# Kernel tuning notes

Hardware: AMD Instinct MI355X
Metric: run time of the kernel (lower is better)

The kernel has to match this reference:

```python
import jax, jax.numpy as jnp
import numpy as np

K = 20
EPS = 1e-5

def get_graph_feature(x, k):
    # x: [B, C, N] -> edge features [B, 2C, N, k]
    xt = jnp.swapaxes(x, 1, 2)  # [B, N, C]
    sq = jnp.sum(xt * xt, axis=-1)  # [B, N]
    # negative squared distance: -(|a|^2 + |b|^2 - 2 a.b)
    pair = 2.0 * jnp.einsum('bnc,bmc->bnm', xt, xt) - sq[:, :, None] - sq[:, None, :]
    idx = jax.lax.top_k(pair, k)[1]  # [B, N, k] nearest neighbors (incl. self)
    neigh = jax.vmap(lambda f, i: f[i])(xt, idx)  # [B, N, k, C]
    ctr = xt[:, :, None, :]  # [B, N, 1, C]
    edge = jnp.concatenate([neigh - ctr, jnp.broadcast_to(ctr, neigh.shape)], axis=-1)  # [B,N,k,2C]
    return jnp.transpose(edge, (0, 3, 1, 2))  # [B, 2C, N, k]

def bn_lrelu(y, g, b, axes):
    # training-mode batchnorm (biased batch stats) + LeakyReLU(0.2)
    m = jnp.mean(y, axis=axes, keepdims=True)
    v = jnp.var(y, axis=axes, keepdims=True)
    shape = [1, -1] + [1] * (y.ndim - 2)
    yn = (y - m) / jnp.sqrt(v + EPS) * g.reshape(shape) + b.reshape(shape)
    return jnp.where(yn >= 0, yn, 0.2 * yn)

def edge_block(x, w, g, b, k):
    e = get_graph_feature(x, k)           # [B, 2C, N, k]
    y = jnp.einsum('bcnk,oc->bonk', e, w)  # 1x1 conv2d, no bias
    y = bn_lrelu(y, g, b, (0, 2, 3))
    return jnp.max(y, axis=-1)            # max over k -> [B, O, N]

def setup_inputs() -> dict:
    key = jax.random.key(0)
    ks = jax.random.split(key, 8)
    B, N = 8, 1024
    num_features = 256
    def w(k_, o, i):
        return jax.random.normal(k_, (o, i), dtype=jnp.float32) * (1.0 / np.sqrt(i))
    d = {
        'x': jax.random.normal(ks[0], (B, N, 3), dtype=jnp.float32),
        'w1': w(ks[1], 64, 6),   'g1': jnp.ones(64),  'b1': jnp.zeros(64),
        'w2': w(ks[2], 64, 128), 'g2': jnp.ones(64),  'b2': jnp.zeros(64),
        'w3': w(ks[3], 128, 128),'g3': jnp.ones(128), 'b3': jnp.zeros(128),
        'w4': w(ks[4], 256, 256),'g4': jnp.ones(256), 'b4': jnp.zeros(256),
        'w5': w(ks[5], 512, 512),'g5': jnp.ones(512), 'b5': jnp.zeros(512),
        'wemb': w(ks[6], num_features, 512),
    }
    return d

def reference(x, w1, g1, b1, w2, g2, b2, w3, g3, b3, w4, g4, b4, w5, g5, b5, wemb):
    xc = jnp.swapaxes(x, 2, 1)  # [B, 3, N]
    x1 = edge_block(xc, w1, g1, b1, K)  # [B, 64, N]
    x2 = edge_block(x1, w2, g2, b2, K)  # [B, 64, N]
    x3 = edge_block(x2, w3, g3, b3, K)  # [B, 128, N]
    x4 = edge_block(x3, w4, g4, b4, K)  # [B, 256, N]
    cat = jnp.concatenate([x1, x2, x3, x4], axis=1)  # [B, 512, N]
    y = jnp.einsum('bcn,oc->bon', cat, w5)            # 1x1 conv1d
    y = bn_lrelu(y, g5, b5, (0, 2))
    feat = jnp.max(y, axis=-1)  # [B, 512]
    return feat @ wemb.T        # [B, num_features]
```

## Files before the change

### kernel.cpp

```cpp
#include <hip/hip_runtime.h>
#include <hip/hip_bf16.h>
#include <math.h>

#define BB 8
#define NN 1024
#define KNNK 20
#define LDC 512

typedef __attribute__((ext_vector_type(8))) short bfrag8;
typedef __attribute__((ext_vector_type(4))) float facc4;
typedef __attribute__((ext_vector_type(2))) float v2f;

struct bh8 { __hip_bfloat16 h[8]; };

__device__ __forceinline__ bh8 cvt8(float4 a, float4 b) {
    bh8 v;
    v.h[0] = __float2bfloat16(a.x); v.h[1] = __float2bfloat16(a.y);
    v.h[2] = __float2bfloat16(a.z); v.h[3] = __float2bfloat16(a.w);
    v.h[4] = __float2bfloat16(b.x); v.h[5] = __float2bfloat16(b.y);
    v.h[6] = __float2bfloat16(b.z); v.h[7] = __float2bfloat16(b.w);
    return v;
}

template<int CTRL, int RMASK>
__device__ __forceinline__ float fmax_dpp(float x) {
    int xi = __float_as_int(x);
    int yi = __builtin_amdgcn_update_dpp(xi, xi, CTRL, RMASK, 0xF, false);
    return fmaxf(x, __int_as_float(yi));
}

__device__ __forceinline__ float wave_max64(float x) {
    x = fmax_dpp<0x121, 0xF>(x);
    x = fmax_dpp<0x122, 0xF>(x);
    x = fmax_dpp<0x124, 0xF>(x);
    x = fmax_dpp<0x128, 0xF>(x);
    x = fmax_dpp<0x142, 0xA>(x);
    x = fmax_dpp<0x143, 0xC>(x);
    return __int_as_float(__builtin_amdgcn_readlane(__float_as_int(x), 63));
}

__device__ __forceinline__ void select20_pf(float (*dist)[1024],
                                            int q0, int w, int lane,
                                            int* __restrict__ idxout) {
    float d[2][16];
    int   sl[2][16];
#pragma unroll
    for (int qi = 0; qi < 2; qi++) {
        int row = w * 2 + qi;
#pragma unroll
        for (int j = 0; j < 16; j++) { d[qi][j] = dist[row][lane + 64 * j]; sl[qi][j] = j; }
    }
    constexpr unsigned char CA[63] = {
        0,2,4,6,8,10,12,14,
        0,1,4,5,8,9,12,13,
        1,5,9,13,
        0,1,2,3,8,9,10,11,
        2,3,10,11,
        1,3,5,9,11,13,
        0,1,2,3,4,5,6,7,
        4,5,6,7,
        2,3,6,7,10,11,
        1,3,5,7,9,11,13};
    constexpr unsigned char CB[63] = {
        1,3,5,7,9,11,13,15,
        2,3,6,7,10,11,14,15,
        2,6,10,14,
        4,5,6,7,12,13,14,15,
        4,5,12,13,
        2,4,6,10,12,14,
        8,9,10,11,12,13,14,15,
        8,9,10,11,
        4,5,8,9,12,13,
        2,4,6,8,10,12,14};
#pragma unroll
    for (int c = 0; c < 63; c++) {
        const int a = CA[c], bq = CB[c];
#pragma unroll
        for (int qi = 0; qi < 2; qi++) {
            bool sw = d[qi][a] < d[qi][bq];
            float dmx = sw ? d[qi][bq] : d[qi][a];
            float dmn = sw ? d[qi][a]  : d[qi][bq];
            d[qi][a] = dmx; d[qi][bq] = dmn;
            int smx = sw ? sl[qi][bq] : sl[qi][a];
            int smn = sw ? sl[qi][a]  : sl[qi][bq];
            sl[qi][a] = smx; sl[qi][bq] = smn;
        }
    }
    unsigned long long slp[2];
#pragma unroll
    for (int qi = 0; qi < 2; qi++) {
        int row = w * 2 + qi;
#pragma unroll
        for (int j = 0; j < 16; j++) dist[row][j * 64 + lane] = d[qi][j];
        unsigned long long p = 0;
#pragma unroll
        for (int j = 0; j < 16; j++) p |= (unsigned long long)sl[qi][j] << (4 * j);
        slp[qi] = p;
    }
    float head[2] = {d[0][0], d[1][0]};
    float pf[2]   = {d[0][1], d[1][1]};
    int   ptr[2]  = {2, 2};
    for (int t = 0; t < KNNK; t++) {
#pragma unroll
        for (int qi = 0; qi < 2; qi++) {
            int row = w * 2 + qi;
            float bv = wave_max64(head[qi]);
            unsigned long long ball = __ballot(head[qi] == bv);
            int wl = (int)__builtin_ctzll(ball);
            bool win = (lane == wl);
            if (win) {
                idxout[(q0 + row) * KNNK + t] = (int)(slp[qi] & 15ull) * 64 + lane;
            }
            head[qi] = win ? pf[qi] : head[qi];
            slp[qi]  = win ? (slp[qi] >> 4) : slp[qi];
            if (win) {
                int p = ptr[qi];
                pf[qi] = (p < 16) ? dist[row][p * 64 + lane] : -INFINITY;
                ptr[qi] = p + 1;
            }
        }
    }
}

__device__ __forceinline__ void zero_r1(float* r1s, float* r1q, int O, int tid) {
    for (int i = tid; i < 32 * O; i += 256) { r1s[i] = 0.f; r1q[i] = 0.f; }
}

__global__ __launch_bounds__(256, 4) void knn3_fused(const float* __restrict__ x,
                                                     const float* __restrict__ w1,
                                                     float* __restrict__ zf,
                                                     int* __restrict__ idxout,
                                                     float* __restrict__ r1s, float* __restrict__ r1q) {
    __shared__ float dist[8][1024];
    int tid = threadIdx.x;
    int q0 = (blockIdx.x & 7) * 1024 + (blockIdx.x >> 3) * 8;
    int b = q0 >> 10;
    if (blockIdx.x == 0) zero_r1(r1s, r1q, 64, tid);
    const float* xb = x + (size_t)b * NN * 3;
    int lane = tid & 63, w = tid >> 6;
    float qx[8], qy[8], qz[8];
#pragma unroll
    for (int q = 0; q < 8; q++) {
        const float* qr = xb + (size_t)((q0 & (NN - 1)) + q) * 3;
        qx[q] = qr[0]; qy[q] = qr[1]; qz[q] = qr[2];
    }
#pragma unroll
    for (int cq = 0; cq < 4; cq++) {
        int cand = w * 256 + cq * 64 + lane;
        const float* cr = xb + (size_t)cand * 3;
        float cx = cr[0], cy = cr[1], cz = cr[2];
        float sqc = cx * cx + cy * cy + cz * cz;
#pragma unroll
        for (int q = 0; q < 8; q++) {
            float d = qx[q] * cx + qy[q] * cy + qz[q] * cz;
            dist[q][cand] = 2.f * d - sqc;
        }
    }
    for (int i = tid; i < 8 * 128; i += 256) {
        int lq = i >> 7, j = i & 127;
        const float* wr = w1 + (j < 64 ? j * 6 : (j - 64) * 6 + 3);
        const float* xr = x + (size_t)(q0 + lq) * 3;
        zf[(size_t)(q0 + lq) * 128 + j] = wr[0] * xr[0] + wr[1] * xr[1] + wr[2] * xr[2];
    }
    __syncthreads();
    select20_pf(dist, q0, w, lane, idxout);
}

template<int C>
__device__ __forceinline__ void knn_body(const float* __restrict__ xT,
                                         const float* __restrict__ sqn,
                                         int* __restrict__ idxout,
                                         float (*dist)[1024], int knnBlk) {
    int tid = threadIdx.x;
    int q0 = (knnBlk & 7) * 1024 + (knnBlk >> 3) * 8;
    int b = q0 >> 10;
    int lane = tid & 63, w = tid >> 6;
    int cand0 = w * 256 + 4 * lane;
    const float* xTb = xT + (size_t)b * C * 1024;
    const float* qrow = xTb + (q0 & (NN - 1));
    float4 sq4 = *(const float4*)(sqn + b * NN + cand0);
    v2f acc2[4][4];
#pragma unroll
    for (int j = 0; j < 4; j++)
#pragma unroll
        for (int p = 0; p < 4; p++) acc2[j][p] = (v2f){0.f, 0.f};
    for (int cg = 0; cg < C / 4; cg++) {
        float4 rch[4];
#pragma unroll
        for (int c = 0; c < 4; c++)
            rch[c] = *(const float4*)(xTb + (size_t)(4 * cg + c) * 1024 + cand0);
#pragma unroll
        for (int c = 0; c < 4; c++) {
            const float* qr = qrow + (size_t)(4 * cg + c) * 1024;
            float4 qa = *(const float4*)qr;
            float4 qb = *(const float4*)(qr + 4);
            v2f qp[4] = {{qa.x, qa.y}, {qa.z, qa.w}, {qb.x, qb.y}, {qb.z, qb.w}};
            float rj[4] = {rch[c].x, rch[c].y, rch[c].z, rch[c].w};
#pragma unroll
            for (int j = 0; j < 4; j++) {
                v2f rr = {rj[j], rj[j]};
                acc2[j][0] += rr * qp[0];
                acc2[j][1] += rr * qp[1];
                acc2[j][2] += rr * qp[2];
                acc2[j][3] += rr * qp[3];
            }
        }
    }
#pragma unroll
    for (int p = 0; p < 4; p++)
#pragma unroll
        for (int half = 0; half < 2; half++) {
            int q = 2 * p + half;
            float4 dv;
            dv.x = 2.f * acc2[0][p][half] - sq4.x;
            dv.y = 2.f * acc2[1][p][half] - sq4.y;
            dv.z = 2.f * acc2[2][p][half] - sq4.z;
            dv.w = 2.f * acc2[3][p][half] - sq4.w;
            *(float4*)&dist[q][cand0] = dv;
        }
    __syncthreads();
    select20_pf(dist, q0, w, lane, idxout);
}

template<int C, int ZO2>
__global__ __launch_bounds__(256, 4) void knnz_fat(const float* __restrict__ xT,
                                                   const float* __restrict__ xt, int off,
                                                   const float* __restrict__ sqn,
                                                   int* __restrict__ idxout,
                                                   const float* __restrict__ w,
                                                   float* __restrict__ zf,
                                                   float* __restrict__ r1s, float* __restrict__ r1q,
                                                   int Onext) {
    __shared__ float dist[8][1024];
    int tid = threadIdx.x;
    if ((int)blockIdx.x < BB * NN / 8) {
        knn_body<C>(xT, sqn, idxout, dist, blockIdx.x);
        return;
    }
    constexpr int ZO = ZO2 / 2;
    int zblk = blockIdx.x - BB * NN / 8;
    if (zblk == 0) zero_r1(r1s, r1q, Onext, tid);
    float (*xs)[C] = (float (*)[C])&dist[0][0];
    int p0 = zblk * 16;
    for (int j = tid; j < 16 * (C / 4); j += 256) {
        int p = j / (C / 4), c4 = j % (C / 4);
        *(float4*)&xs[p][4 * c4] = *(const float4*)(xt + (size_t)(p0 + p) * LDC + off + 4 * c4);
    }
    __syncthreads();
    for (int j = tid; j < ZO2; j += 256) {
        const float* wr = w + (j < ZO ? (size_t)j * 2 * C : (size_t)(j - ZO) * 2 * C + C);
        float acc[16];
#pragma unroll
        for (int p = 0; p < 16; p++) acc[p] = 0.f;
        for (int c4 = 0; c4 < C / 4; c4++) {
            float4 wv = *(const float4*)(wr + 4 * c4);
#pragma unroll
            for (int p = 0; p < 16; p++) {
                float4 xv = *(const float4*)&xs[p][4 * c4];
                acc[p] += wv.x * xv.x + wv.y * xv.y + wv.z * xv.z + wv.w * xv.w;
            }
        }
#pragma unroll
        for (int p = 0; p < 16; p++) zf[(size_t)(p0 + p) * ZO2 + j] = acc[p];
    }
}

__global__ __launch_bounds__(256, 4) void knnz4_fat(const float* __restrict__ xT,
                                                    const float* __restrict__ sqn,
                                                    int* __restrict__ idxout,
                                                    const float* __restrict__ xtcat,
                                                    const float* __restrict__ w4,
                                                    __hip_bfloat16* __restrict__ zf4,
                                                    float* __restrict__ r1s, float* __restrict__ r1q) {
    __shared__ __align__(16) char smem[36864];
    int tid = threadIdx.x;
    if ((int)blockIdx.x < BB * NN / 8) {
        float (*dist)[1024] = (float (*)[1024])smem;
        if (blockIdx.x == 0) zero_r1(r1s, r1q, 256, tid);
        knn_body<128>(xT, sqn, idxout, dist, blockIdx.x);
        return;
    }
    __hip_bfloat16 (*A)[72] = (__hip_bfloat16 (*)[72])smem;
    __hip_bfloat16 (*W)[72] = (__hip_bfloat16 (*)[72])(smem + 18432);
    int zblk = blockIdx.x - BB * NN / 8;
    int mt = zblk >> 2, nt = zblk & 3;
    int lane = tid & 63, wvx = tid >> 6;
    int mw = wvx >> 1, nw = wvx & 1;
    int m0 = lane & 15, qd = lane >> 4;
    int r = tid & 127, hf = tid >> 7;
    facc4 acc[4][4];
    facc4 zz = {0.f, 0.f, 0.f, 0.f};
#pragma unroll
    for (int mi = 0; mi < 4; mi++)
#pragma unroll
        for (int ni = 0; ni < 4; ni++) acc[mi][ni] = zz;
    int j = nt * 128 + r;
    const float* wsrc = w4 + (j < 256 ? (size_t)j * 256 : (size_t)(j - 256) * 256 + 128);
    const float* asrc = xtcat + (size_t)(mt * 128 + r) * 512 + 128;
    for (int kc = 0; kc < 2; kc++) {
#pragma unroll
        for (int u = 0; u < 4; u++) {
            int c0 = kc * 64 + hf * 32 + 8 * u;
            float4 a0 = *(const float4*)(asrc + c0);
            float4 a1 = *(const float4*)(asrc + c0 + 4);
            *(bh8*)&A[r][hf * 32 + 8 * u] = cvt8(a0, a1);
            float4 w0 = *(const float4*)(wsrc + c0);
            float4 w1 = *(const float4*)(wsrc + c0 + 4);
            *(bh8*)&W[r][hf * 32 + 8 * u] = cvt8(w0, w1);
        }
        __syncthreads();
#pragma unroll
        for (int kk = 0; kk < 2; kk++) {
            bfrag8 af[4], bf[4];
#pragma unroll
            for (int mi = 0; mi < 4; mi++)
                af[mi] = *(const bfrag8*)&A[64 * mw + 16 * mi + m0][32 * kk + 8 * qd];
#pragma unroll
            for (int ni = 0; ni < 4; ni++)
                bf[ni] = *(const bfrag8*)&W[64 * nw + 16 * ni + m0][32 * kk + 8 * qd];
#pragma unroll
            for (int mi = 0; mi < 4; mi++)
#pragma unroll
                for (int ni = 0; ni < 4; ni++)
                    acc[mi][ni] = __builtin_amdgcn_mfma_f32_16x16x32_bf16(af[mi], bf[ni], acc[mi][ni], 0, 0, 0);
        }
        __syncthreads();
    }
#pragma unroll
    for (int mi = 0; mi < 4; mi++)
#pragma unroll
        for (int ni = 0; ni < 4; ni++)
#pragma unroll
            for (int rg = 0; rg < 4; rg++) {
                int row = mt * 128 + mw * 64 + mi * 16 + qd * 4 + rg;
                int col = nt * 128 + nw * 64 + ni * 16 + m0;
                zf4[(size_t)row * 512 + col] = __float2bfloat16(acc[mi][ni][rg]);
            }
}

template<int O2>
__global__ __launch_bounds__(256) void gatherstats_k(const float* __restrict__ zf,
                                                     const int* __restrict__ idx,
                                                     float* __restrict__ ymax, float* __restrict__ ymin,
                                                     float* __restrict__ r1s, float* __restrict__ r1q) {
    constexpr int O = O2 / 2;
    __shared__ float red_s[4][O], red_q[4][O];
    int wv = threadIdx.x >> 6, lane = threadIdx.x & 63;
    int n = (blockIdx.x & 7) * 1024 + (blockIdx.x >> 3) * 4 + wv;
    int b = n >> 10;
    const float* zbatch = zf + (size_t)b * NN * O2;
    int nb[KNNK];
#pragma unroll
    for (int k = 0; k < KNNK; k++) nb[k] = idx[n * KNNK + k];
#pragma unroll
    for (int ch = 0; ch < O / 64; ch++) {
        int o = ch * 64 + lane;
        float g[KNNK];
#pragma unroll
        for (int k = 0; k < KNNK; k++) g[k] = zbatch[(size_t)nb[k] * O2 + o];
        float mx = -INFINITY, mn = INFINITY, s = 0.f, ss = 0.f;
#pragma unroll
        for (int k = 0; k < KNNK; k++) {
            float v = g[k];
            mx = fmaxf(mx, v); mn = fminf(mn, v); s += v; ss += v * v;
        }
        float zn  = zf[(size_t)n * O2 + o];
        float zbn = zf[(size_t)n * O2 + O + o];
        float d = zbn - zn;
        mx += d; mn += d;
        ss = ss + 2.f * d * s + (float)KNNK * d * d;
        s  = s + (float)KNNK * d;
        ymax[(size_t)n * O + o] = mx;
        ymin[(size_t)n * O + o] = mn;
        red_s[wv][o] = s;
        red_q[wv][o] = ss;
    }
    __syncthreads();
    int bucket = blockIdx.x & 31;
    for (int o = threadIdx.x; o < O; o += 256) {
        float s4 = red_s[0][o] + red_s[1][o] + red_s[2][o] + red_s[3][o];
        float q4 = red_q[0][o] + red_q[1][o] + red_q[2][o] + red_q[3][o];
        atomicAdd(&r1s[(size_t)bucket * O + o], s4);
        atomicAdd(&r1q[(size_t)bucket * O + o], q4);
    }
}

__global__ __launch_bounds__(256) void gatherstats4_k(const __hip_bfloat16* __restrict__ zf4,
                                                      const int* __restrict__ idx,
                                                      float* __restrict__ ymax, float* __restrict__ ymin,
                                                      float* __restrict__ r1s, float* __restrict__ r1q) {
    __shared__ float red_s[4][256], red_q[4][256];
    int wv = threadIdx.x >> 6, lane = threadIdx.x & 63;
    int n = (blockIdx.x & 7) * 1024 + (blockIdx.x >> 3) * 4 + wv;
    int b = n >> 10;
    const __hip_bfloat16* zbatch = zf4 + (size_t)b * NN * 512;
    int nb[KNNK];
#pragma unroll
    for (int k = 0; k < KNNK; k++) nb[k] = idx[n * KNNK + k];
#pragma unroll
    for (int ch = 0; ch < 4; ch++) {
        int o = ch * 64 + lane;
        float g[KNNK];
#pragma unroll
        for (int k = 0; k < KNNK; k++) g[k] = __bfloat162float(zbatch[(size_t)nb[k] * 512 + o]);
        float mx = -INFINITY, mn = INFINITY, s = 0.f, ss = 0.f;
#pragma unroll
        for (int k = 0; k < KNNK; k++) {
            float v = g[k];
            mx = fmaxf(mx, v); mn = fminf(mn, v); s += v; ss += v * v;
        }
        float zn  = __bfloat162float(zf4[(size_t)n * 512 + o]);
        float zbn = __bfloat162float(zf4[(size_t)n * 512 + 256 + o]);
        float d = zbn - zn;
        mx += d; mn += d;
        ss = ss + 2.f * d * s + (float)KNNK * d * d;
        s  = s + (float)KNNK * d;
        ymax[(size_t)n * 256 + o] = mx;
        ymin[(size_t)n * 256 + o] = mn;
        red_s[wv][o] = s;
        red_q[wv][o] = ss;
    }
    __syncthreads();
    int bucket = blockIdx.x & 31;
    for (int o = threadIdx.x; o < 256; o += 256) {
        float s4 = red_s[0][o] + red_s[1][o] + red_s[2][o] + red_s[3][o];
        float q4 = red_q[0][o] + red_q[1][o] + red_q[2][o] + red_q[3][o];
        atomicAdd(&r1s[(size_t)bucket * 256 + o], s4);
        atomicAdd(&r1q[(size_t)bucket * 256 + o], q4);
    }
}

template<int O>
__global__ __launch_bounds__(256) void epitrans2_k(const float* __restrict__ ymax, const float* __restrict__ ymin,
                                                   const float* __restrict__ r1s, const float* __restrict__ r1q,
                                                   const float* __restrict__ g, const float* __restrict__ beta,
                                                   double invM,
                                                   float* __restrict__ xtcat, int off_out,
                                                   float* __restrict__ xT, float* __restrict__ sqn,
                                                   __hip_bfloat16* __restrict__ xbf) {
    __shared__ float tile[64][O + 1];
    __shared__ float ssh[O], tth[O];
    int n0 = blockIdx.x * 64;
    int b = n0 >> 10;
    int tid = threadIdx.x;
    for (int o = tid; o < O; o += 256) {
        double sd = 0.0, qd = 0.0;
        for (int r = 0; r < 32; r++) { sd += r1s[(size_t)r * O + o]; qd += r1q[(size_t)r * O + o]; }
        double mean = sd * invM;
        double var = qd * invM - mean * mean;
        float inv = (float)(1.0 / sqrt(var + 1e-5));
        float sc = g[o] * inv;
        ssh[o] = sc;
        tth[o] = beta[o] - (float)mean * sc;
    }
    __syncthreads();
    for (int i = tid; i < 64 * O; i += 256) {
        int nl = i / O;
        int o = i & (O - 1);
        int n = n0 + nl;
        float sc = ssh[o];
        float v = sc >= 0.f ? ymax[(size_t)n * O + o] : ymin[(size_t)n * O + o];
        float y = sc * v + tth[o];
        y = y >= 0.f ? y : 0.2f * y;
        xtcat[(size_t)n * LDC + off_out + o] = y;
        xbf[(size_t)n * LDC + off_out + o] = __float2bfloat16(y);
        tile[nl][o] = y;
    }
    __syncthreads();
    if (tid < 64) {
        float sq = 0.f;
        for (int c = 0; c < O; c++) { float v = tile[tid][c]; sq += v * v; }
        sqn[n0 + tid] = sq;
    }
    int r = tid >> 4, cq = tid & 15;
#pragma unroll
    for (int ct = 0; ct < O / 16; ct++) {
        int c = ct * 16 + r;
        float4 ov;
        ov.x = tile[4 * cq + 0][c];
        ov.y = tile[4 * cq + 1][c];
        ov.z = tile[4 * cq + 2][c];
        ov.w = tile[4 * cq + 3][c];
        *(float4*)(xT + ((size_t)b * O + c) * 1024 + (n0 & (NN - 1)) + 4 * cq) = ov;
    }
}

__global__ __launch_bounds__(256) void epilogue4_k(const float* __restrict__ ymax, const float* __restrict__ ymin,
                                                   const float* __restrict__ r1s, const float* __restrict__ r1q,
                                                   const float* __restrict__ g, const float* __restrict__ beta,
                                                   double invM,
                                                   __hip_bfloat16* __restrict__ xbf) {
    __shared__ float ssh[256], tth[256];
    int n0 = blockIdx.x * 32;
    int tid = threadIdx.x;
    {
        int o = tid;
        double sd = 0.0, qd = 0.0;
        for (int r = 0; r < 32; r++) { sd += r1s[(size_t)r * 256 + o]; qd += r1q[(size_t)r * 256 + o]; }
        double mean = sd * invM;
        double var = qd * invM - mean * mean;
        float inv = (float)(1.0 / sqrt(var + 1e-5));
        float sc = g[o] * inv;
        ssh[o] = sc;
        tth[o] = beta[o] - (float)mean * sc;
    }
    __syncthreads();
    for (int i = tid; i < 32 * 256; i += 256) {
        int nl = i >> 8;
        int o = i & 255;
        int n = n0 + nl;
        float sc = ssh[o];
        float v = sc >= 0.f ? ymax[(size_t)n * 256 + o] : ymin[(size_t)n * 256 + o];
        float y = sc * v + tth[o];
        y = y >= 0.f ? y : 0.2f * y;
        xbf[(size_t)n * LDC + 256 + o] = __float2bfloat16(y);
    }
}

__global__ __launch_bounds__(256) void gemm5_mfma(const __hip_bfloat16* __restrict__ xbf,
                                                  const float* __restrict__ w5,
                                                  float* __restrict__ pmax, float* __restrict__ pmn,
                                                  float* __restrict__ ps, float* __restrict__ pq) {
    __shared__ __hip_bfloat16 A[128][72];
    __shared__ __hip_bfloat16 W[128][72];
    int mt = blockIdx.x >> 2, nt = blockIdx.x & 3;
    int tid = threadIdx.x;
    int lane = tid & 63, wvx = tid >> 6;
    int mw = wvx >> 1, nw = wvx & 1;
    int m0 = lane & 15, qd = lane >> 4;
    int r = tid & 127, hf = tid >> 7;
    facc4 acc[4][4];
    facc4 zz = {0.f, 0.f, 0.f, 0.f};
#pragma unroll
    for (int mi = 0; mi < 4; mi++)
#pragma unroll
        for (int ni = 0; ni < 4; ni++) acc[mi][ni] = zz;
    for (int kc = 0; kc < 8; kc++) {
        const __hip_bfloat16* ap = xbf + (size_t)(mt * 128 + r) * 512 + kc * 64 + hf * 32;
        const float* wp = w5 + (size_t)(nt * 128 + r) * 512 + kc * 64 + hf * 32;
#pragma unroll
        for (int u = 0; u < 4; u++) {
            bh8 av = *(const bh8*)(ap + 8 * u);
            *(bh8*)&A[r][hf * 32 + 8 * u] = av;
            float4 w0 = *(const float4*)(wp + 8 * u);
            float4 w1 = *(const float4*)(wp + 8 * u + 4);
            *(bh8*)&W[r][hf * 32 + 8 * u] = cvt8(w0, w1);
        }
        __syncthreads();
#pragma unroll
        for (int kk = 0; kk < 2; kk++) {
            bfrag8 af[4], bf[4];
#pragma unroll
            for (int mi = 0; mi < 4; mi++)
                af[mi] = *(const bfrag8*)&A[64 * mw + 16 * mi + m0][32 * kk + 8 * qd];
#pragma unroll
            for (int ni = 0; ni < 4; ni++)
                bf[ni] = *(const bfrag8*)&W[64 * nw + 16 * ni + m0][32 * kk + 8 * qd];
#pragma unroll
            for (int mi = 0; mi < 4; mi++)
#pragma unroll
                for (int ni = 0; ni < 4; ni++)
                    acc[mi][ni] = __builtin_amdgcn_mfma_f32_16x16x32_bf16(af[mi], bf[ni], acc[mi][ni], 0, 0, 0);
        }
        __syncthreads();
    }
#pragma unroll
    for (int mi = 0; mi < 4; mi++) {
        int grp = mt * 8 + mw * 4 + mi;
#pragma unroll
        for (int ni = 0; ni < 4; ni++) {
            float mx = -INFINITY, mn = INFINITY, s = 0.f, ss = 0.f;
#pragma unroll
            for (int rg = 0; rg < 4; rg++) {
                float v = acc[mi][ni][rg];
                mx = fmaxf(mx, v); mn = fminf(mn, v); s += v; ss += v * v;
            }
#pragma unroll
            for (int m = 16; m < 64; m <<= 1) {
                mx = fmaxf(mx, __shfl_xor(mx, m));
                mn = fminf(mn, __shfl_xor(mn, m));
                s += __shfl_xor(s, m);
                ss += __shfl_xor(ss, m);
            }
            if (qd == 0) {
                int o = nt * 128 + nw * 64 + ni * 16 + m0;
                pmax[(size_t)grp * 512 + o] = mx;
                pmn [(size_t)grp * 512 + o] = mn;
                ps  [(size_t)grp * 512 + o] = s;
                pq  [(size_t)grp * 512 + o] = ss;
            }
        }
    }
}

__global__ __launch_bounds__(256) void bnstat5_k(const float* __restrict__ ps, const float* __restrict__ pq,
                                                 const float* __restrict__ g, const float* __restrict__ beta,
                                                 float* __restrict__ s_out, float* __restrict__ t_out) {
    __shared__ double lds_s[4][8], lds_q[4][8];
    int tid = threadIdx.x;
    int lane = tid & 63, wv = tid >> 6;
    int ol = lane & 7;
    int rg = wv * 8 + (lane >> 3);
    int o = blockIdx.x * 8 + ol;
    double s = 0.0, q = 0.0;
    for (int r = rg; r < 512; r += 32) {
        s += ps[(size_t)r * 512 + o];
        q += pq[(size_t)r * 512 + o];
    }
    s += __shfl_xor(s, 8);  q += __shfl_xor(q, 8);
    s += __shfl_xor(s, 16); q += __shfl_xor(q, 16);
    s += __shfl_xor(s, 32); q += __shfl_xor(q, 32);
    if (lane < 8) { lds_s[wv][ol] = s; lds_q[wv][ol] = q; }
    __syncthreads();
    if (tid < 8) {
        s = lds_s[0][tid] + lds_s[1][tid] + lds_s[2][tid] + lds_s[3][tid];
        q = lds_q[0][tid] + lds_q[1][tid] + lds_q[2][tid] + lds_q[3][tid];
        double invM = 1.0 / (BB * NN);
        double mean = s * invM;
        double var = q * invM - mean * mean;
        float inv = (float)(1.0 / sqrt(var + 1e-5));
        int oo = blockIdx.x * 8 + tid;
        float sc = g[oo] * inv;
        s_out[oo] = sc;
        t_out[oo] = beta[oo] - (float)mean * sc;
    }
}

__global__ __launch_bounds__(256) void featreduce_k(const float* __restrict__ pmax, const float* __restrict__ pmn,
                                                    const float* __restrict__ s, const float* __restrict__ t,
                                                    float* __restrict__ feat8) {
    __shared__ float smx[4][64], smn[4][64];
    int blk = blockIdx.x;
    int b = blk >> 3, oc = blk & 7;
    int tid = threadIdx.x;
    int lane = tid & 63, wv = tid >> 6;
    int o = oc * 64 + lane;
    float mx = -INFINITY, mn = INFINITY;
    for (int r = b * 64 + wv; r < (b + 1) * 64; r += 4) {
        mx = fmaxf(mx, pmax[(size_t)r * 512 + o]);
        mn = fminf(mn, pmn [(size_t)r * 512 + o]);
    }
    smx[wv][lane] = mx; smn[wv][lane] = mn;
    __syncthreads();
    if (wv == 0) {
        mx = fmaxf(fmaxf(smx[0][lane], smx[1][lane]), fmaxf(smx[2][lane], smx[3][lane]));
        mn = fminf(fminf(smn[0][lane], smn[1][lane]), fminf(smn[2][lane], smn[3][lane]));
        float sc = s[o];
        float v = sc >= 0.f ? mx : mn;
        float y = sc * v + t[o];
        feat8[(size_t)b * 512 + o] = y >= 0.f ? y : 0.2f * y;
    }
}

__global__ __launch_bounds__(256) void outgemm_k(const float* __restrict__ feat8,
                                                 const float* __restrict__ wemb,
                                                 float* __restrict__ out) {
    __shared__ __align__(16) float feat[512];
    int blk = blockIdx.x;
    int b = blk >> 3, nc = blk & 7;
    int tid = threadIdx.x;
    for (int i = tid; i < 512; i += 256) feat[i] = feat8[(size_t)b * 512 + i];
    __syncthreads();
    int o_l = tid >> 3, kc = tid & 7;
    int o = nc * 32 + o_l;
    const float4* wr = (const float4*)(wemb + (size_t)o * 512 + kc * 64);
    const float4* fv = (const float4*)(feat + kc * 64);
    float acc = 0.f;
#pragma unroll
    for (int i = 0; i < 16; i++) {
        float4 wv = wr[i];
        float4 f  = fv[i];
        acc += wv.x * f.x + wv.y * f.y + wv.z * f.z + wv.w * f.w;
    }
    acc += __shfl_xor(acc, 1);
    acc += __shfl_xor(acc, 2);
    acc += __shfl_xor(acc, 4);
    if (kc == 0) out[(size_t)b * 256 + o] = acc;
}

extern "C" void kernel_launch(void* const* d_in, const int* in_sizes, int n_in,
                              void* d_out, int out_size, void* d_ws, size_t ws_size,
                              hipStream_t stream) {
    const float* x    = (const float*)d_in[0];
    const float* w1   = (const float*)d_in[1];
    const float* g1   = (const float*)d_in[2];
    const float* b1   = (const float*)d_in[3];
    const float* w2   = (const float*)d_in[4];
    const float* g2   = (const float*)d_in[5];
    const float* b2   = (const float*)d_in[6];
    const float* w3   = (const float*)d_in[7];
    const float* g3   = (const float*)d_in[8];
    const float* b3   = (const float*)d_in[9];
    const float* w4   = (const float*)d_in[10];
    const float* g4   = (const float*)d_in[11];
    const float* b4   = (const float*)d_in[12];
    const float* w5   = (const float*)d_in[13];
    const float* g5   = (const float*)d_in[14];
    const float* b5   = (const float*)d_in[15];
    const float* wemb = (const float*)d_in[16];
    float* out = (float*)d_out;

    float* fws    = (float*)d_ws;
    float* xtcat  = fws;
    float* ymax   = xtcat + (size_t)BB * NN * 512;
    float* ymin   = ymax + (size_t)BB * NN * 256;
    float* psum   = ymin + (size_t)BB * NN * 256;
    float* psumsq = psum + (size_t)BB * NN * 256;
    float* xT     = psum;
    float* pmax   = ymax;
    float* pmn    = pmax + 512 * 512;
    float* ps5    = pmn + 512 * 512;
    float* pq5    = ps5 + 512 * 512;
    float* feat8  = psumsq;
    float* sqn    = psumsq + (size_t)BB * NN * 256;
    float* s_arr  = sqn + BB * NN;
    float* t_arr  = s_arr + 512;
    float* r1s    = t_arr + 512;
    float* r1q    = r1s + 32 * 512;
    int*   idxb   = (int*)(r1q + 32 * 512);
    float* zfull  = (float*)(idxb + BB * NN * KNNK);
    __hip_bfloat16* zf4 = (__hip_bfloat16*)zfull;
    __hip_bfloat16* xbf = (__hip_bfloat16*)(zfull + (size_t)BB * NN * 512);

    const double invM_edge = 1.0 / ((double)BB * NN * KNNK);
    const int nbn = BB * NN;
    const int NK = nbn / 8;
    const int NZ = nbn / 16;

    knn3_fused<<<NK, 256, 0, stream>>>(x, w1, zfull, idxb, r1s, r1q);
    gatherstats_k<128><<<nbn / 4, 256, 0, stream>>>(zfull, idxb, ymax, ymin, r1s, r1q);
    epitrans2_k<64><<<128, 256, 0, stream>>>(ymax, ymin, r1s, r1q, g1, b1, invM_edge, xtcat, 0, xT, sqn, xbf);

    knnz_fat<64, 128><<<NK + NZ, 256, 0, stream>>>(xT, xtcat, 0, sqn, idxb, w2, zfull, r1s, r1q, 64);
    gatherstats_k<128><<<nbn / 4, 256, 0, stream>>>(zfull, idxb, ymax, ymin, r1s, r1q);
    epitrans2_k<64><<<128, 256, 0, stream>>>(ymax, ymin, r1s, r1q, g2, b2, invM_edge, xtcat, 64, xT, sqn, xbf);

    knnz_fat<64, 256><<<NK + NZ, 256, 0, stream>>>(xT, xtcat, 64, sqn, idxb, w3, zfull, r1s, r1q, 128);
    gatherstats_k<256><<<nbn / 4, 256, 0, stream>>>(zfull, idxb, ymax, ymin, r1s, r1q);
    epitrans2_k<128><<<128, 256, 0, stream>>>(ymax, ymin, r1s, r1q, g3, b3, invM_edge, xtcat, 128, xT, sqn, xbf);

    knnz4_fat<<<NK + 256, 256, 0, stream>>>(xT, sqn, idxb, xtcat, w4, zf4, r1s, r1q);
    gatherstats4_k<<<nbn / 4, 256, 0, stream>>>(zf4, idxb, ymax, ymin, r1s, r1q);
    epilogue4_k<<<256, 256, 0, stream>>>(ymax, ymin, r1s, r1q, g4, b4, invM_edge, xbf);

    gemm5_mfma<<<256, 256, 0, stream>>>(xbf, w5, pmax, pmn, ps5, pq5);
    bnstat5_k<<<64, 256, 0, stream>>>(ps5, pq5, g5, b5, s_arr, t_arr);
    featreduce_k<<<64, 256, 0, stream>>>(pmax, pmn, s_arr, t_arr, feat8);
    outgemm_k<<<64, 256, 0, stream>>>(feat8, wemb, out);
}
```

Baseline: 326.1 us.

## Process 16 queries per KNN block with per-wave four-query top-k selection

The KNN blocks in the layer-2 to layer-4 kernels now compute distances for 16 query points instead of 8. Each candidate load is reused across twice as many queries, and half as many blocks reread the candidate features. A new selection routine handles four query rows per wave, and the distance buffer in shared memory doubles to 64 KB. Launch bounds drop from 4 to 2 blocks per CU, which cuts occupancy and grid parallelism and adds register pressure from the larger accumulator array.

```diff
diff --git a/kernel.cpp b/kernel.cpp
--- a/kernel.cpp
+++ b/kernel.cpp
@@ -21,6 +21,29 @@
     v.h[6] = __float2bfloat16(b.z); v.h[7] = __float2bfloat16(b.w);
     return v;
 }
+
+static constexpr unsigned char s_CA[63] = {
+    0,2,4,6,8,10,12,14,
+    0,1,4,5,8,9,12,13,
+    1,5,9,13,
+    0,1,2,3,8,9,10,11,
+    2,3,10,11,
+    1,3,5,9,11,13,
+    0,1,2,3,4,5,6,7,
+    4,5,6,7,
+    2,3,6,7,10,11,
+    1,3,5,7,9,11,13};
+static constexpr unsigned char s_CB[63] = {
+    1,3,5,7,9,11,13,15,
+    2,3,6,7,10,11,14,15,
+    2,6,10,14,
+    4,5,6,7,12,13,14,15,
+    4,5,12,13,
+    2,4,6,10,12,14,
+    8,9,10,11,12,13,14,15,
+    8,9,10,11,
+    4,5,8,9,12,13,
+    2,4,6,8,10,12,14};
 
 template<int CTRL, int RMASK>
 __device__ __forceinline__ float fmax_dpp(float x) {
@@ -50,31 +73,9 @@
 #pragma unroll
         for (int j = 0; j < 16; j++) { d[qi][j] = dist[row][lane + 64 * j]; sl[qi][j] = j; }
     }
-    constexpr unsigned char CA[63] = {
-        0,2,4,6,8,10,12,14,
-        0,1,4,5,8,9,12,13,
-        1,5,9,13,
-        0,1,2,3,8,9,10,11,
-        2,3,10,11,
-        1,3,5,9,11,13,
-        0,1,2,3,4,5,6,7,
-        4,5,6,7,
-        2,3,6,7,10,11,
-        1,3,5,7,9,11,13};
-    constexpr unsigned char CB[63] = {
-        1,3,5,7,9,11,13,15,
-        2,3,6,7,10,11,14,15,
-        2,6,10,14,
-        4,5,6,7,12,13,14,15,
-        4,5,12,13,
-        2,4,6,10,12,14,
-        8,9,10,11,12,13,14,15,
-        8,9,10,11,
-        4,5,8,9,12,13,
-        2,4,6,8,10,12,14};
 #pragma unroll
     for (int c = 0; c < 63; c++) {
-        const int a = CA[c], bq = CB[c];
+        const int a = s_CA[c], bq = s_CB[c];
 #pragma unroll
         for (int qi = 0; qi < 2; qi++) {
             bool sw = d[qi][a] < d[qi][bq];
@@ -122,6 +123,62 @@
     }
 }
 
+__device__ __forceinline__ void select20_q4(float (*dist)[1024],
+                                            int q0, int w, int lane,
+                                            int* __restrict__ idxout) {
+    unsigned long long slp[4];
+    float head[4], pf[4];
+    int   ptr[4];
+#pragma unroll
+    for (int qi = 0; qi < 4; qi++) {
+        int row = w * 4 + qi;
+        float d[16];
+        int   sl[16];
+#pragma unroll
+        for (int j = 0; j < 16; j++) { d[j] = dist[row][lane + 64 * j]; sl[j] = j; }
+#pragma unroll
+        for (int c = 0; c < 63; c++) {
+            const int a = s_CA[c], bq = s_CB[c];
+            bool sw = d[a] < d[bq];
+            float dmx = sw ? d[bq] : d[a];
+            float dmn = sw ? d[a]  : d[bq];
+            d[a] = dmx; d[bq] = dmn;
+            int smx = sw ? sl[bq] : sl[a];
+            int smn = sw ? sl[a]  : sl[bq];
+            sl[a] = smx; sl[bq] = smn;
+        }
+#pragma unroll
+        for (int j = 0; j < 16; j++) dist[row][j * 64 + lane] = d[j];
+        unsigned long long p = 0;
+#pragma unroll
+        for (int j = 0; j < 16; j++) p |= (unsigned long long)sl[j] << (4 * j);
+        slp[qi]  = p;
+        head[qi] = d[0];
+        pf[qi]   = d[1];
+        ptr[qi]  = 2;
+    }
+    for (int t = 0; t < KNNK; t++) {
+#pragma unroll
+        for (int qi = 0; qi < 4; qi++) {
+            int row = w * 4 + qi;
+            float bv = wave_max64(head[qi]);
+            unsigned long long ball = __ballot(head[qi] == bv);
+            int wl = (int)__builtin_ctzll(ball);
+            bool win = (lane == wl);
+            if (win) {
+                idxout[(q0 + row) * KNNK + t] = (int)(slp[qi] & 15ull) * 64 + lane;
+            }
+            head[qi] = win ? pf[qi] : head[qi];
+            slp[qi]  = win ? (slp[qi] >> 4) : slp[qi];
+            if (win) {
+                int p = ptr[qi];
+                pf[qi] = (p < 16) ? dist[row][p * 64 + lane] : -INFINITY;
+                ptr[qi] = p + 1;
+            }
+        }
+    }
+}
+
 __device__ __forceinline__ void zero_r1(float* r1s, float* r1q, int O, int tid) {
     for (int i = tid; i < 32 * O; i += 256) { r1s[i] = 0.f; r1q[i] = 0.f; }
 }
@@ -167,23 +224,23 @@
 }
 
 template<int C>
-__device__ __forceinline__ void knn_body(const float* __restrict__ xT,
-                                         const float* __restrict__ sqn,
-                                         int* __restrict__ idxout,
-                                         float (*dist)[1024], int knnBlk) {
-    int tid = threadIdx.x;
-    int q0 = (knnBlk & 7) * 1024 + (knnBlk >> 3) * 8;
+__device__ __forceinline__ void knn_body16(const float* __restrict__ xT,
+                                           const float* __restrict__ sqn,
+                                           int* __restrict__ idxout,
+                                           float (*dist)[1024], int knnBlk) {
+    int tid = threadIdx.x;
+    int q0 = (knnBlk & 7) * 1024 + (knnBlk >> 3) * 16;
     int b = q0 >> 10;
     int lane = tid & 63, w = tid >> 6;
     int cand0 = w * 256 + 4 * lane;
     const float* xTb = xT + (size_t)b * C * 1024;
     const float* qrow = xTb + (q0 & (NN - 1));
     float4 sq4 = *(const float4*)(sqn + b * NN + cand0);
-    v2f acc2[4][4];
+    v2f acc2[4][8];
 #pragma unroll
     for (int j = 0; j < 4; j++)
 #pragma unroll
-        for (int p = 0; p < 4; p++) acc2[j][p] = (v2f){0.f, 0.f};
+        for (int p = 0; p < 8; p++) acc2[j][p] = (v2f){0.f, 0.f};
     for (int cg = 0; cg < C / 4; cg++) {
         float4 rch[4];
 #pragma unroll
@@ -194,20 +251,21 @@
             const float* qr = qrow + (size_t)(4 * cg + c) * 1024;
             float4 qa = *(const float4*)qr;
             float4 qb = *(const float4*)(qr + 4);
-            v2f qp[4] = {{qa.x, qa.y}, {qa.z, qa.w}, {qb.x, qb.y}, {qb.z, qb.w}};
+            float4 qc = *(const float4*)(qr + 8);
+            float4 qd = *(const float4*)(qr + 12);
+            v2f qp[8] = {{qa.x, qa.y}, {qa.z, qa.w}, {qb.x, qb.y}, {qb.z, qb.w},
+                         {qc.x, qc.y}, {qc.z, qc.w}, {qd.x, qd.y}, {qd.z, qd.w}};
             float rj[4] = {rch[c].x, rch[c].y, rch[c].z, rch[c].w};
 #pragma unroll
             for (int j = 0; j < 4; j++) {
                 v2f rr = {rj[j], rj[j]};
-                acc2[j][0] += rr * qp[0];
-                acc2[j][1] += rr * qp[1];
-                acc2[j][2] += rr * qp[2];
-                acc2[j][3] += rr * qp[3];
-            }
-        }
-    }
-#pragma unroll
-    for (int p = 0; p < 4; p++)
+#pragma unroll
+                for (int p = 0; p < 8; p++) acc2[j][p] += rr * qp[p];
+            }
+        }
+    }
+#pragma unroll
+    for (int p = 0; p < 8; p++)
 #pragma unroll
         for (int half = 0; half < 2; half++) {
             int q = 2 * p + half;
@@ -219,11 +277,11 @@
             *(float4*)&dist[q][cand0] = dv;
         }
     __syncthreads();
-    select20_pf(dist, q0, w, lane, idxout);
+    select20_q4(dist, q0, w, lane, idxout);
 }
 
 template<int C, int ZO2>
-__global__ __launch_bounds__(256, 4) void knnz_fat(const float* __restrict__ xT,
+__global__ __launch_bounds__(256, 2) void knnz_fat(const float* __restrict__ xT,
                                                    const float* __restrict__ xt, int off,
                                                    const float* __restrict__ sqn,
                                                    int* __restrict__ idxout,
@@ -231,14 +289,14 @@
                                                    float* __restrict__ zf,
                                                    float* __restrict__ r1s, float* __restrict__ r1q,
                                                    int Onext) {
-    __shared__ float dist[8][1024];
-    int tid = threadIdx.x;
-    if ((int)blockIdx.x < BB * NN / 8) {
-        knn_body<C>(xT, sqn, idxout, dist, blockIdx.x);
+    __shared__ float dist[16][1024];
+    int tid = threadIdx.x;
+    if ((int)blockIdx.x < BB * NN / 16) {
+        knn_body16<C>(xT, sqn, idxout, dist, blockIdx.x);
         return;
     }
     constexpr int ZO = ZO2 / 2;
-    int zblk = blockIdx.x - BB * NN / 8;
+    int zblk = blockIdx.x - BB * NN / 16;
     if (zblk == 0) zero_r1(r1s, r1q, Onext, tid);
     float (*xs)[C] = (float (*)[C])&dist[0][0];
     int p0 = zblk * 16;
@@ -265,24 +323,24 @@
     }
 }
 
-__global__ __launch_bounds__(256, 4) void knnz4_fat(const float* __restrict__ xT,
+__global__ __launch_bounds__(256, 2) void knnz4_fat(const float* __restrict__ xT,
                                                     const float* __restrict__ sqn,
                                                     int* __restrict__ idxout,
                                                     const float* __restrict__ xtcat,
                                                     const float* __restrict__ w4,
                                                     __hip_bfloat16* __restrict__ zf4,
                                                     float* __restrict__ r1s, float* __restrict__ r1q) {
-    __shared__ __align__(16) char smem[36864];
-    int tid = threadIdx.x;
-    if ((int)blockIdx.x < BB * NN / 8) {
+    __shared__ __align__(16) char smem[65536];
+    int tid = threadIdx.x;
+    if ((int)blockIdx.x < BB * NN / 16) {
         float (*dist)[1024] = (float (*)[1024])smem;
         if (blockIdx.x == 0) zero_r1(r1s, r1q, 256, tid);
-        knn_body<128>(xT, sqn, idxout, dist, blockIdx.x);
+        knn_body16<128>(xT, sqn, idxout, dist, blockIdx.x);
         return;
     }
     __hip_bfloat16 (*A)[72] = (__hip_bfloat16 (*)[72])smem;
     __hip_bfloat16 (*W)[72] = (__hip_bfloat16 (*)[72])(smem + 18432);
-    int zblk = blockIdx.x - BB * NN / 8;
+    int zblk = blockIdx.x - BB * NN / 16;
     int mt = zblk >> 2, nt = zblk & 3;
     int lane = tid & 63, wvx = tid >> 6;
     int mw = wvx >> 1, nw = wvx & 1;
@@ -724,22 +782,23 @@
 
     const double invM_edge = 1.0 / ((double)BB * NN * KNNK);
     const int nbn = BB * NN;
-    const int NK = nbn / 8;
-    const int NZ = nbn / 16;
+    const int NK  = nbn / 8;
+    const int NK16 = nbn / 16;
+    const int NZ  = nbn / 16;
 
     knn3_fused<<<NK, 256, 0, stream>>>(x, w1, zfull, idxb, r1s, r1q);
     gatherstats_k<128><<<nbn / 4, 256, 0, stream>>>(zfull, idxb, ymax, ymin, r1s, r1q);
     epitrans2_k<64><<<128, 256, 0, stream>>>(ymax, ymin, r1s, r1q, g1, b1, invM_edge, xtcat, 0, xT, sqn, xbf);
 
-    knnz_fat<64, 128><<<NK + NZ, 256, 0, stream>>>(xT, xtcat, 0, sqn, idxb, w2, zfull, r1s, r1q, 64);
+    knnz_fat<64, 128><<<NK16 + NZ, 256, 0, stream>>>(xT, xtcat, 0, sqn, idxb, w2, zfull, r1s, r1q, 64);
     gatherstats_k<128><<<nbn / 4, 256, 0, stream>>>(zfull, idxb, ymax, ymin, r1s, r1q);
     epitrans2_k<64><<<128, 256, 0, stream>>>(ymax, ymin, r1s, r1q, g2, b2, invM_edge, xtcat, 64, xT, sqn, xbf);
 
-    knnz_fat<64, 256><<<NK + NZ, 256, 0, stream>>>(xT, xtcat, 64, sqn, idxb, w3, zfull, r1s, r1q, 128);
+    knnz_fat<64, 256><<<NK16 + NZ, 256, 0, stream>>>(xT, xtcat, 64, sqn, idxb, w3, zfull, r1s, r1q, 128);
     gatherstats_k<256><<<nbn / 4, 256, 0, stream>>>(zfull, idxb, ymax, ymin, r1s, r1q);
     epitrans2_k<128><<<128, 256, 0, stream>>>(ymax, ymin, r1s, r1q, g3, b3, invM_edge, xtcat, 128, xT, sqn, xbf);
 
-    knnz4_fat<<<NK + 256, 256, 0, stream>>>(xT, sqn, idxb, xtcat, w4, zf4, r1s, r1q);
+    knnz4_fat<<<NK16 + 256, 256, 0, stream>>>(xT, sqn, idxb, xtcat, w4, zf4, r1s, r1q);
     gatherstats4_k<<<nbn / 4, 256, 0, stream>>>(zf4, idxb, ymax, ymin, r1s, r1q);
     epilogue4_k<<<256, 256, 0, stream>>>(ymax, ymin, r1s, r1q, g4, b4, invM_edge, xbf);
 
```

New measurement: 476.5 us. 46.1% more time.

## Process 16 queries per KNN block with 512 threads to reuse candidate loads

Applied to the files above, without the earlier changes.

The KNN distance phase now handles 16 query points per block with 512 threads instead of 8 queries with 256 threads. Each thread covers 2 candidates across 16 queries, so every candidate feature load feeds twice as many FMAs. This also halves the number of KNN blocks launched. The fused Z-projection blocks are launched at the larger block size too. Their extra threads are either masked out or repeat strided loops that were written for 256 threads, which wastes work. The LDS footprint doubles to 64KB, which may reduce how many blocks can be resident at once.

```diff
diff --git a/kernel.cpp b/kernel.cpp
--- a/kernel.cpp
+++ b/kernel.cpp
@@ -167,63 +167,60 @@
 }
 
 template<int C>
-__device__ __forceinline__ void knn_body(const float* __restrict__ xT,
-                                         const float* __restrict__ sqn,
-                                         int* __restrict__ idxout,
-                                         float (*dist)[1024], int knnBlk) {
-    int tid = threadIdx.x;
-    int q0 = (knnBlk & 7) * 1024 + (knnBlk >> 3) * 8;
+__device__ __forceinline__ void knn_body16w(const float* __restrict__ xT,
+                                            const float* __restrict__ sqn,
+                                            int* __restrict__ idxout,
+                                            float (*dist)[1024], int knnBlk) {
+    int tid = threadIdx.x;
+    int q0 = (knnBlk & 7) * 1024 + (knnBlk >> 3) * 16;
     int b = q0 >> 10;
     int lane = tid & 63, w = tid >> 6;
-    int cand0 = w * 256 + 4 * lane;
+    int cand0 = 2 * tid;
     const float* xTb = xT + (size_t)b * C * 1024;
     const float* qrow = xTb + (q0 & (NN - 1));
-    float4 sq4 = *(const float4*)(sqn + b * NN + cand0);
-    v2f acc2[4][4];
-#pragma unroll
-    for (int j = 0; j < 4; j++)
-#pragma unroll
-        for (int p = 0; p < 4; p++) acc2[j][p] = (v2f){0.f, 0.f};
-    for (int cg = 0; cg < C / 4; cg++) {
-        float4 rch[4];
-#pragma unroll
-        for (int c = 0; c < 4; c++)
-            rch[c] = *(const float4*)(xTb + (size_t)(4 * cg + c) * 1024 + cand0);
-#pragma unroll
-        for (int c = 0; c < 4; c++) {
-            const float* qr = qrow + (size_t)(4 * cg + c) * 1024;
+    float2 sq2 = *(const float2*)(sqn + b * NN + cand0);
+    v2f acc2[8][2];
+#pragma unroll
+    for (int k = 0; k < 8; k++) { acc2[k][0] = (v2f){0.f, 0.f}; acc2[k][1] = (v2f){0.f, 0.f}; }
+    for (int cg = 0; cg < C / 8; cg++) {
+        float2 rch[8];
+#pragma unroll
+        for (int c = 0; c < 8; c++)
+            rch[c] = *(const float2*)(xTb + (size_t)(8 * cg + c) * 1024 + cand0);
+#pragma unroll
+        for (int c = 0; c < 8; c++) {
+            const float* qr = qrow + (size_t)(8 * cg + c) * 1024;
             float4 qa = *(const float4*)qr;
             float4 qb = *(const float4*)(qr + 4);
-            v2f qp[4] = {{qa.x, qa.y}, {qa.z, qa.w}, {qb.x, qb.y}, {qb.z, qb.w}};
-            float rj[4] = {rch[c].x, rch[c].y, rch[c].z, rch[c].w};
-#pragma unroll
-            for (int j = 0; j < 4; j++) {
-                v2f rr = {rj[j], rj[j]};
-                acc2[j][0] += rr * qp[0];
-                acc2[j][1] += rr * qp[1];
-                acc2[j][2] += rr * qp[2];
-                acc2[j][3] += rr * qp[3];
-            }
-        }
-    }
-#pragma unroll
-    for (int p = 0; p < 4; p++)
+            float4 qc = *(const float4*)(qr + 8);
+            float4 qd = *(const float4*)(qr + 12);
+            v2f qp[8] = {{qa.x, qa.y}, {qa.z, qa.w}, {qb.x, qb.y}, {qb.z, qb.w},
+                         {qc.x, qc.y}, {qc.z, qc.w}, {qd.x, qd.y}, {qd.z, qd.w}};
+            v2f r0 = {rch[c].x, rch[c].x};
+            v2f r1 = {rch[c].y, rch[c].y};
+#pragma unroll
+            for (int k = 0; k < 8; k++) {
+                acc2[k][0] += qp[k] * r0;
+                acc2[k][1] += qp[k] * r1;
+            }
+        }
+    }
+#pragma unroll
+    for (int k = 0; k < 8; k++)
 #pragma unroll
         for (int half = 0; half < 2; half++) {
-            int q = 2 * p + half;
-            float4 dv;
-            dv.x = 2.f * acc2[0][p][half] - sq4.x;
-            dv.y = 2.f * acc2[1][p][half] - sq4.y;
-            dv.z = 2.f * acc2[2][p][half] - sq4.z;
-            dv.w = 2.f * acc2[3][p][half] - sq4.w;
-            *(float4*)&dist[q][cand0] = dv;
+            int q = 2 * k + half;
+            float2 dv;
+            dv.x = 2.f * acc2[k][0][half] - sq2.x;
+            dv.y = 2.f * acc2[k][1][half] - sq2.y;
+            *(float2*)&dist[q][cand0] = dv;
         }
     __syncthreads();
     select20_pf(dist, q0, w, lane, idxout);
 }
 
 template<int C, int ZO2>
-__global__ __launch_bounds__(256, 4) void knnz_fat(const float* __restrict__ xT,
+__global__ __launch_bounds__(512, 4) void knnz_fat(const float* __restrict__ xT,
                                                    const float* __restrict__ xt, int off,
                                                    const float* __restrict__ sqn,
                                                    int* __restrict__ idxout,
@@ -231,14 +228,14 @@
                                                    float* __restrict__ zf,
                                                    float* __restrict__ r1s, float* __restrict__ r1q,
                                                    int Onext) {
-    __shared__ float dist[8][1024];
-    int tid = threadIdx.x;
-    if ((int)blockIdx.x < BB * NN / 8) {
-        knn_body<C>(xT, sqn, idxout, dist, blockIdx.x);
+    __shared__ float dist[16][1024];
+    int tid = threadIdx.x;
+    if ((int)blockIdx.x < BB * NN / 16) {
+        knn_body16w<C>(xT, sqn, idxout, dist, blockIdx.x);
         return;
     }
     constexpr int ZO = ZO2 / 2;
-    int zblk = blockIdx.x - BB * NN / 8;
+    int zblk = blockIdx.x - BB * NN / 16;
     if (zblk == 0) zero_r1(r1s, r1q, Onext, tid);
     float (*xs)[C] = (float (*)[C])&dist[0][0];
     int p0 = zblk * 16;
@@ -265,29 +262,30 @@
     }
 }
 
-__global__ __launch_bounds__(256, 4) void knnz4_fat(const float* __restrict__ xT,
+__global__ __launch_bounds__(512, 4) void knnz4_fat(const float* __restrict__ xT,
                                                     const float* __restrict__ sqn,
                                                     int* __restrict__ idxout,
                                                     const float* __restrict__ xtcat,
                                                     const float* __restrict__ w4,
                                                     __hip_bfloat16* __restrict__ zf4,
                                                     float* __restrict__ r1s, float* __restrict__ r1q) {
-    __shared__ __align__(16) char smem[36864];
-    int tid = threadIdx.x;
-    if ((int)blockIdx.x < BB * NN / 8) {
+    __shared__ __align__(16) char smem[65536];
+    int tid = threadIdx.x;
+    if ((int)blockIdx.x < BB * NN / 16) {
         float (*dist)[1024] = (float (*)[1024])smem;
         if (blockIdx.x == 0) zero_r1(r1s, r1q, 256, tid);
-        knn_body<128>(xT, sqn, idxout, dist, blockIdx.x);
+        knn_body16w<128>(xT, sqn, idxout, dist, blockIdx.x);
         return;
     }
     __hip_bfloat16 (*A)[72] = (__hip_bfloat16 (*)[72])smem;
     __hip_bfloat16 (*W)[72] = (__hip_bfloat16 (*)[72])(smem + 18432);
-    int zblk = blockIdx.x - BB * NN / 8;
+    bool zact = tid < 256;
+    int zblk = blockIdx.x - BB * NN / 16;
     int mt = zblk >> 2, nt = zblk & 3;
     int lane = tid & 63, wvx = tid >> 6;
-    int mw = wvx >> 1, nw = wvx & 1;
+    int mw = (wvx >> 1) & 1, nw = wvx & 1;
     int m0 = lane & 15, qd = lane >> 4;
-    int r = tid & 127, hf = tid >> 7;
+    int r = tid & 127, hf = (tid >> 7) & 1;
     facc4 acc[4][4];
     facc4 zz = {0.f, 0.f, 0.f, 0.f};
 #pragma unroll
@@ -298,44 +296,50 @@
     const float* wsrc = w4 + (j < 256 ? (size_t)j * 256 : (size_t)(j - 256) * 256 + 128);
     const float* asrc = xtcat + (size_t)(mt * 128 + r) * 512 + 128;
     for (int kc = 0; kc < 2; kc++) {
-#pragma unroll
-        for (int u = 0; u < 4; u++) {
-            int c0 = kc * 64 + hf * 32 + 8 * u;
-            float4 a0 = *(const float4*)(asrc + c0);
-            float4 a1 = *(const float4*)(asrc + c0 + 4);
-            *(bh8*)&A[r][hf * 32 + 8 * u] = cvt8(a0, a1);
-            float4 w0 = *(const float4*)(wsrc + c0);
-            float4 w1 = *(const float4*)(wsrc + c0 + 4);
-            *(bh8*)&W[r][hf * 32 + 8 * u] = cvt8(w0, w1);
+        if (zact) {
+#pragma unroll
+            for (int u = 0; u < 4; u++) {
+                int c0 = kc * 64 + hf * 32 + 8 * u;
+                float4 a0 = *(const float4*)(asrc + c0);
+                float4 a1 = *(const float4*)(asrc + c0 + 4);
+                *(bh8*)&A[r][hf * 32 + 8 * u] = cvt8(a0, a1);
+                float4 w0 = *(const float4*)(wsrc + c0);
+                float4 w1 = *(const float4*)(wsrc + c0 + 4);
+                *(bh8*)&W[r][hf * 32 + 8 * u] = cvt8(w0, w1);
+            }
         }
         __syncthreads();
-#pragma unroll
-        for (int kk = 0; kk < 2; kk++) {
-            bfrag8 af[4], bf[4];
-#pragma unroll
-            for (int mi = 0; mi < 4; mi++)
-                af[mi] = *(const bfrag8*)&A[64 * mw + 16 * mi + m0][32 * kk + 8 * qd];
+        if (zact) {
+#pragma unroll
+            for (int kk = 0; kk < 2; kk++) {
+                bfrag8 af[4], bf[4];
+#pragma unroll
+                for (int mi = 0; mi < 4; mi++)
+                    af[mi] = *(const bfrag8*)&A[64 * mw + 16 * mi + m0][32 * kk + 8 * qd];
+#pragma unroll
+                for (int ni = 0; ni < 4; ni++)
+                    bf[ni] = *(const bfrag8*)&W[64 * nw + 16 * ni + m0][32 * kk + 8 * qd];
+#pragma unroll
+                for (int mi = 0; mi < 4; mi++)
+#pragma unroll
+                    for (int ni = 0; ni < 4; ni++)
+                        acc[mi][ni] = __builtin_amdgcn_mfma_f32_16x16x32_bf16(af[mi], bf[ni], acc[mi][ni], 0, 0, 0);
+            }
+        }
+        __syncthreads();
+    }
+    if (zact) {
+#pragma unroll
+        for (int mi = 0; mi < 4; mi++)
 #pragma unroll
             for (int ni = 0; ni < 4; ni++)
-                bf[ni] = *(const bfrag8*)&W[64 * nw + 16 * ni + m0][32 * kk + 8 * qd];
-#pragma unroll
-            for (int mi = 0; mi < 4; mi++)
-#pragma unroll
-                for (int ni = 0; ni < 4; ni++)
-                    acc[mi][ni] = __builtin_amdgcn_mfma_f32_16x16x32_bf16(af[mi], bf[ni], acc[mi][ni], 0, 0, 0);
-        }
-        __syncthreads();
-    }
-#pragma unroll
-    for (int mi = 0; mi < 4; mi++)
-#pragma unroll
-        for (int ni = 0; ni < 4; ni++)
-#pragma unroll
-            for (int rg = 0; rg < 4; rg++) {
-                int row = mt * 128 + mw * 64 + mi * 16 + qd * 4 + rg;
-                int col = nt * 128 + nw * 64 + ni * 16 + m0;
-                zf4[(size_t)row * 512 + col] = __float2bfloat16(acc[mi][ni][rg]);
-            }
+#pragma unroll
+                for (int rg = 0; rg < 4; rg++) {
+                    int row = mt * 128 + mw * 64 + mi * 16 + qd * 4 + rg;
+                    int col = nt * 128 + nw * 64 + ni * 16 + m0;
+                    zf4[(size_t)row * 512 + col] = __float2bfloat16(acc[mi][ni][rg]);
+                }
+    }
 }
 
 template<int O2>
@@ -724,22 +728,23 @@
 
     const double invM_edge = 1.0 / ((double)BB * NN * KNNK);
     const int nbn = BB * NN;
-    const int NK = nbn / 8;
-    const int NZ = nbn / 16;
+    const int NK   = nbn / 8;
+    const int NK16 = nbn / 16;
+    const int NZ   = nbn / 16;
 
     knn3_fused<<<NK, 256, 0, stream>>>(x, w1, zfull, idxb, r1s, r1q);
     gatherstats_k<128><<<nbn / 4, 256, 0, stream>>>(zfull, idxb, ymax, ymin, r1s, r1q);
     epitrans2_k<64><<<128, 256, 0, stream>>>(ymax, ymin, r1s, r1q, g1, b1, invM_edge, xtcat, 0, xT, sqn, xbf);
 
-    knnz_fat<64, 128><<<NK + NZ, 256, 0, stream>>>(xT, xtcat, 0, sqn, idxb, w2, zfull, r1s, r1q, 64);
+    knnz_fat<64, 128><<<NK16 + NZ, 512, 0, stream>>>(xT, xtcat, 0, sqn, idxb, w2, zfull, r1s, r1q, 64);
     gatherstats_k<128><<<nbn / 4, 256, 0, stream>>>(zfull, idxb, ymax, ymin, r1s, r1q);
     epitrans2_k<64><<<128, 256, 0, stream>>>(ymax, ymin, r1s, r1q, g2, b2, invM_edge, xtcat, 64, xT, sqn, xbf);
 
-    knnz_fat<64, 256><<<NK + NZ, 256, 0, stream>>>(xT, xtcat, 64, sqn, idxb, w3, zfull, r1s, r1q, 128);
+    knnz_fat<64, 256><<<NK16 + NZ, 512, 0, stream>>>(xT, xtcat, 64, sqn, idxb, w3, zfull, r1s, r1q, 128);
     gatherstats_k<256><<<nbn / 4, 256, 0, stream>>>(zfull, idxb, ymax, ymin, r1s, r1q);
     epitrans2_k<128><<<128, 256, 0, stream>>>(ymax, ymin, r1s, r1q, g3, b3, invM_edge, xtcat, 128, xT, sqn, xbf);
 
-    knnz4_fat<<<NK + 256, 256, 0, stream>>>(xT, sqn, idxb, xtcat, w4, zf4, r1s, r1q);
+    knnz4_fat<<<NK16 + 256, 512, 0, stream>>>(xT, sqn, idxb, xtcat, w4, zf4, r1s, r1q);
     gatherstats4_k<<<nbn / 4, 256, 0, stream>>>(zf4, idxb, ymax, ymin, r1s, r1q);
     epilogue4_k<<<256, 256, 0, stream>>>(ymax, ymin, r1s, r1q, g4, b4, invM_edge, xbf);
 
```

After: 319.2 us. 2.1% less time.
